# Kernel tuning notes

Hardware: AMD Instinct MI355X
Metric: run time of the kernel (lower is better)

Reference implementation:

```python
import jax, jax.numpy as jnp
import numpy as np

B, S, DM = 1, 2048, 2048
H, KV, DH = 32, 8, 64
ROT, DQ = 32, 16  # rotary dims; DQ = ROT // 2
GROUPS = H // KV


def setup_inputs() -> dict:
    key = jax.random.key(0)
    ks = jax.random.split(key, 9)
    sc = 0.02
    hidden_states = jax.random.normal(ks[0], (B, S, DM), jnp.float32)
    # realistic RoPE tables: theta = pos * inv_freq, shape [1,1,S,DQ] (broadcasts over heads)
    inv_freq = 1.0 / (10000.0 ** (jnp.arange(DQ, dtype=jnp.float32) / DQ))
    ang = jnp.arange(S, dtype=jnp.float32)[:, None] * inv_freq[None, :]
    cos = jnp.cos(ang)[None, None]
    sin = jnp.sin(ang)[None, None]
    position_ids = jnp.broadcast_to(jnp.arange(S, dtype=jnp.int64 if jax.config.read('jax_enable_x64') else jnp.int32), (B, S))
    Wq = jax.random.normal(ks[1], (DM, H * DH), jnp.float32) * sc
    Wk = jax.random.normal(ks[2], (DM, KV * DH), jnp.float32) * sc
    Wv = jax.random.normal(ks[3], (DM, KV * DH), jnp.float32) * sc
    Wo = jax.random.normal(ks[4], (H * DH, DM), jnp.float32) * sc
    qkv_dim = H * DH + 2 * KV * DH
    tau_Wq = jax.random.normal(ks[5], (qkv_dim, H), jnp.float32) * sc
    tau_Wv = jax.random.normal(ks[6], (qkv_dim, H), jnp.float32) * sc
    tau_alpha = jax.random.normal(ks[7], (H,), jnp.float32)
    return {"hidden_states": hidden_states, "cos": cos, "sin": sin,
            "position_ids": position_ids, "Wq": Wq, "Wk": Wk, "Wv": Wv,
            "Wo": Wo, "tau_Wq": tau_Wq, "tau_Wv": tau_Wv, "tau_alpha": tau_alpha}


def _rope(x, cos, sin):
    # x: [B, h, S, DH]; rotate first ROT dims (half-split real/imag), interleave output
    x_rot, x_pass = x[..., :ROT], x[..., ROT:]
    xr, xi = x_rot[..., :DQ], x_rot[..., DQ:]
    out_r = xr * cos - xi * sin
    out_i = xr * sin + xi * cos
    out = jnp.stack([out_r, out_i], axis=-1).reshape(x.shape[:-1] + (ROT,))
    return jnp.concatenate([out, x_pass], axis=-1)


def reference(hidden_states, cos, sin, position_ids, Wq, Wk, Wv, Wo, tau_Wq, tau_Wv, tau_alpha):
    b, s, _ = hidden_states.shape
    q = hidden_states @ Wq                      # [B,S,H*DH]
    k = hidden_states @ Wk                      # [B,S,KV*DH]
    v = hidden_states @ Wv                      # [B,S,KV*DH]
    # tau gating: gelu(concat qkv) -> tanh projections -> position sigmoid term
    feat = jax.nn.gelu(jnp.concatenate([q, k, v], axis=-1), approximate=False)
    tok_q = jnp.tanh(feat @ tau_Wq).transpose(0, 2, 1)   # [B,H,S]
    tok_v = jnp.tanh(feat @ tau_Wv).transpose(0, 2, 1)   # [B,H,S]
    pos = position_ids.astype(hidden_states.dtype) + 1.0
    tau_pos = 1.0 + (jax.nn.sigmoid(tau_alpha[None, :, None] * jnp.log(pos)[:, None, :]) - 0.5)
    tau_q = (tok_q + tau_pos)[..., None]        # [B,H,S,1]
    tau_v = (tok_v + tau_pos)[..., None]        # [B,H,S,1]
    q = q.reshape(b, s, H, DH).transpose(0, 2, 1, 3) * tau_q   # [B,H,S,DH]
    k = k.reshape(b, s, KV, DH).transpose(0, 2, 1, 3)          # [B,KV,S,DH]
    # torch: tau_v.repeat(1,groups,1,1)[:, :KV] == first KV heads of tau_v
    v = v.reshape(b, s, KV, DH).transpose(0, 2, 1, 3) * tau_v[:, :KV]
    q = _rope(q, cos, sin)
    k = _rope(k, cos, sin)
    # GQA expand kv heads, causal SDPA
    k = jnp.repeat(k, GROUPS, axis=1)
    v = jnp.repeat(v, GROUPS, axis=1)
    scores = jnp.einsum('bhqd,bhkd->bhqk', q, k) / np.sqrt(DH).astype(np.float32)
    causal = jnp.tril(jnp.ones((s, s), dtype=bool))
    scores = jnp.where(causal, scores, jnp.finfo(scores.dtype).min)
    attn = jax.nn.softmax(scores, axis=-1)
    out = jnp.einsum('bhqk,bhkd->bhqd', attn, v)
    out = out.transpose(0, 2, 1, 3).reshape(b, s, H * DH)
    return out @ Wo
```

## Files before the change

kernel.cpp:

```cpp
#include <hip/hip_runtime.h>
#include <cmath>

typedef __bf16 bf16x8 __attribute__((ext_vector_type(8)));
typedef __bf16 bf16x4 __attribute__((ext_vector_type(4)));
typedef float f32x4 __attribute__((ext_vector_type(4)));
typedef unsigned short u16;
typedef unsigned int u32;

__device__ __forceinline__ u16 f2bf(float f) {
  union { float f; unsigned int u; } v; v.f = f;
  unsigned int u = v.u;
  return (u16)((u + 0x7FFFu + ((u >> 16) & 1u)) >> 16);
}
__device__ __forceinline__ float bf2f(u16 b) {
  union { u32 u; float f; } v; v.u = ((u32)b) << 16; return v.f;
}

__device__ __forceinline__ float geluf(float x) {
  return 0.5f * x * (1.0f + erff(x * 0.7071067811865475f));
}

__device__ __forceinline__ void gl_lds16(const void* g, void* l) {
  __builtin_amdgcn_global_load_lds(
      (const __attribute__((address_space(1))) u32*)g,
      (__attribute__((address_space(3))) u32*)l, 16, 0, 0);
}

__global__ __launch_bounds__(256) void setup_all(const float* __restrict__ hidden,
                                                 const float* __restrict__ Wq,
                                                 const float* __restrict__ Wk,
                                                 const float* __restrict__ Wv,
                                                 const float* __restrict__ Wo,
                                                 const float* __restrict__ tWq,
                                                 const float* __restrict__ tWv,
                                                 u16* __restrict__ Xb,
                                                 u16* __restrict__ WqkvT,
                                                 u16* __restrict__ WoT,
                                                 u16* __restrict__ Tt) {
  __shared__ float tile[64][65];
  int b = blockIdx.x;
  if (b < 2048) {
    int i = b * 256 + threadIdx.x;
    const float4* p = (const float4*)hidden + 2 * (size_t)i;
    float4 a = p[0], c = p[1];
    uint4 o;
    o.x = (u32)f2bf(a.x) | ((u32)f2bf(a.y) << 16);
    o.y = (u32)f2bf(a.z) | ((u32)f2bf(a.w) << 16);
    o.z = (u32)f2bf(c.x) | ((u32)f2bf(c.y) << 16);
    o.w = (u32)f2bf(c.z) | ((u32)f2bf(c.w) << 16);
    ((uint4*)Xb)[i] = o;
    return;
  }
  b -= 2048;
  const float* in; u16* out; int R, C, bx, by;
  if (b < 1024)      { in = Wq;  out = WqkvT;                R = 2048; C = 2048; bx = b & 31; by = b >> 5; }
  else if (b < 1280) { b -= 1024; in = Wk; out = WqkvT + 2048ull * 2048; R = 2048; C = 512; bx = b & 7; by = b >> 3; }
  else if (b < 1536) { b -= 1280; in = Wv; out = WqkvT + 2560ull * 2048; R = 2048; C = 512; bx = b & 7; by = b >> 3; }
  else if (b < 2560) { b -= 1536; in = Wo; out = WoT;        R = 2048; C = 2048; bx = b & 31; by = b >> 5; }
  else if (b < 2608) { b -= 2560; in = tWq; out = Tt;               R = 3072; C = 32; bx = 0; by = b; }
  else               { b -= 2608; in = tWv; out = Tt + 32ull * 3072; R = 3072; C = 32; bx = 0; by = b; }

  const int t = threadIdx.x;
  const int r0 = by * 64, c0 = bx * 64;
  const int lr = t >> 4, lc4 = (t & 15) * 4;
#pragma unroll
  for (int p = 0; p < 4; ++p) {
    int r = p * 16 + lr;
    float4 v = {0.f, 0.f, 0.f, 0.f};
    if (c0 + lc4 < C) v = *(const float4*)(in + (size_t)(r0 + r) * C + c0 + lc4);
    tile[r][lc4] = v.x; tile[r][lc4 + 1] = v.y;
    tile[r][lc4 + 2] = v.z; tile[r][lc4 + 3] = v.w;
  }
  __syncthreads();
  const int cg = t >> 4, rr4 = (t & 15) * 4;
#pragma unroll
  for (int p = 0; p < 4; ++p) {
    int c = p * 16 + cg;
    if (c0 + c < C) {
      uint2 w;
      w.x = (u32)f2bf(tile[rr4][c])     | ((u32)f2bf(tile[rr4 + 1][c]) << 16);
      w.y = (u32)f2bf(tile[rr4 + 2][c]) | ((u32)f2bf(tile[rr4 + 3][c]) << 16);
      *(uint2*)(out + (size_t)(c0 + c) * R + r0 + rr4) = w;
    }
  }
}

template <int WR, int WC, bool ATOMIC>
__global__ __launch_bounds__(256, 3) void gemm_bt(const u16* __restrict__ A,
                                                  const u16* __restrict__ Bt,
                                                  float* __restrict__ Cpart,
                                                  int M, int N, int K, int kPer) {
  constexpr int BM = WR * 64, BN = WC * 64;
  __shared__ __attribute__((aligned(16))) u16 As[BM * 64];
  __shared__ __attribute__((aligned(16))) u16 Bs[BN * 64];
  const int tid = threadIdx.x, wid = tid >> 6, lane = tid & 63;
  const int l16 = lane & 15, quad = lane >> 4;
  const int wm = (wid % WR) * 64, wn = (wid / WR) * 64;
  const int m0 = blockIdx.y * BM, n0 = blockIdx.x * BN;
  const int kIters = K >> 6;
  const int kStart = blockIdx.z * kPer;
  const int kEnd = (kStart + kPer < kIters) ? (kStart + kPer) : kIters;

  const int lrow = lane >> 3;
  const int swz = (lane & 7) ^ lrow;
  const u16* gAb = A + (size_t)m0 * K + (size_t)swz * 8;
  const u16* gBb = Bt + (size_t)n0 * K + (size_t)swz * 8;
  const int sx = l16 & 7;

  f32x4 acc[4][4] = {};
  for (int kt = kStart; kt < kEnd; ++kt) {
    __syncthreads();
    const u16* gA = gAb + (size_t)kt * 64;
    const u16* gB = gBb + (size_t)kt * 64;
#pragma unroll
    for (int j = 0; j < BM / 32; ++j) {
      int i = wid * (BM / 32) + j;
      gl_lds16(gA + (size_t)(i * 8 + lrow) * K, &As[i * 512]);
    }
#pragma unroll
    for (int j = 0; j < BN / 32; ++j) {
      int i = wid * (BN / 32) + j;
      gl_lds16(gB + (size_t)(i * 8 + lrow) * K, &Bs[i * 512]);
    }
    __syncthreads();
    bf16x8 af[4][2], bfr[4][2];
#pragma unroll
    for (int mt = 0; mt < 4; ++mt)
#pragma unroll
      for (int ks = 0; ks < 2; ++ks)
        af[mt][ks] = *(const bf16x8*)(&As[(wm + mt * 16 + l16) * 64 +
                                          (((ks * 4 + quad) ^ sx) * 8)]);
#pragma unroll
    for (int nt = 0; nt < 4; ++nt)
#pragma unroll
      for (int ks = 0; ks < 2; ++ks)
        bfr[nt][ks] = *(const bf16x8*)(&Bs[(wn + nt * 16 + l16) * 64 +
                                           (((ks * 4 + quad) ^ sx) * 8)]);
#pragma unroll
    for (int mt = 0; mt < 4; ++mt)
#pragma unroll
      for (int nt = 0; nt < 4; ++nt)
#pragma unroll
        for (int ks = 0; ks < 2; ++ks)
          acc[mt][nt] = __builtin_amdgcn_mfma_f32_16x16x32_bf16(
              af[mt][ks], bfr[nt][ks], acc[mt][nt], 0, 0, 0);
  }

  float* C = ATOMIC ? Cpart : Cpart + (size_t)blockIdx.z * M * N;
#pragma unroll
  for (int mt = 0; mt < 4; ++mt)
#pragma unroll
    for (int nt = 0; nt < 4; ++nt)
#pragma unroll
      for (int r = 0; r < 4; ++r) {
        int row = m0 + wm + mt * 16 + quad * 4 + r;
        int col = n0 + wn + nt * 16 + l16;
        if constexpr (ATOMIC)
          unsafeAtomicAdd(&C[(size_t)row * N + col], acc[mt][nt][r]);
        else
          C[(size_t)row * N + col] = acc[mt][nt][r];
      }
}

__global__ __launch_bounds__(256) void reduce_gelu(float* __restrict__ base, int P,
                                                   int n4, u16* __restrict__ gout) {
  int i = blockIdx.x * 256 + threadIdx.x;
  if (i >= n4) return;
  size_t n = (size_t)n4 * 4;
  float4 v = ((const float4*)base)[i];
  for (int p = 1; p < P; ++p) {
    float4 w = ((const float4*)(base + (size_t)p * n))[i];
    v.x += w.x; v.y += w.y; v.z += w.z; v.w += w.w;
  }
  if (P > 1) ((float4*)base)[i] = v;
  uint2 o;
  o.x = (u32)f2bf(geluf(v.x)) | ((u32)f2bf(geluf(v.y)) << 16);
  o.y = (u32)f2bf(geluf(v.z)) | ((u32)f2bf(geluf(v.w)) << 16);
  ((uint2*)gout)[i] = o;
}

#define QSCALE 0.18033688011112042f
__global__ __launch_bounds__(256) void prep_qkv(const float* __restrict__ qkv,
                                                const float* __restrict__ tokPart,
                                                int P,
                                                const float* __restrict__ alpha,
                                                const float* __restrict__ cosb,
                                                const float* __restrict__ sinb,
                                                const int* __restrict__ pos_ids,
                                                u16* __restrict__ Qb,
                                                u16* __restrict__ Kb,
                                                u16* __restrict__ Vt,
                                                u16* __restrict__ Vb) {
  const int s = blockIdx.x;
  const int tid = threadIdx.x;
  __shared__ float cs[16], sn[16], tk[64], tq_s[32], tv_s[32];
  if (tid < 16) { cs[tid] = cosb[s * 16 + tid]; sn[tid] = sinb[s * 16 + tid]; }
  if (tid >= 64 && tid < 128) {
    int c = tid - 64;
    float v = 0.f;
    for (int p = 0; p < P; ++p) v += tokPart[(size_t)p * 2048 * 64 + s * 64 + c];
    tk[c] = tanhf(v);
  }
  __syncthreads();
  if (tid < 32) {
    float p = (float)pos_ids[s] + 1.0f;
    float sig = 1.0f / (1.0f + __expf(-alpha[tid] * logf(p)));
    float taupos = 0.5f + sig;
    tq_s[tid] = (tk[tid] + taupos) * QSCALE;
    tv_s[tid] = tk[tid + 32] + taupos;
  }
  __syncthreads();
  const float* row = qkv + (size_t)s * 3072;

  for (int idx = tid; idx < 2048; idx += 256) {
    int h = idx >> 6, d = idx & 63;
    float tq = tq_s[h];
    float v;
    if (d < 32) {
      int i = d >> 1;
      float xr = row[h * 64 + i] * tq, xi = row[h * 64 + 16 + i] * tq;
      v = (d & 1) ? (xr * sn[i] + xi * cs[i]) : (xr * cs[i] - xi * sn[i]);
    } else v = row[h * 64 + d] * tq;
    Qb[((size_t)h * 2048 + s) * 64 + d] = f2bf(v);
  }
  for (int idx = tid; idx < 512; idx += 256) {
    int h = idx >> 6, d = idx & 63;
    const float* kr = row + 2048;
    float v;
    if (d < 32) {
      int i = d >> 1;
      float xr = kr[h * 64 + i], xi = kr[h * 64 + 16 + i];
      v = (d & 1) ? (xr * sn[i] + xi * cs[i]) : (xr * cs[i] - xi * sn[i]);
    } else v = kr[h * 64 + d];
    Kb[((size_t)h * 2048 + s) * 64 + d] = f2bf(v);
  }
  for (int idx = tid; idx < 512; idx += 256) {
    int h = idx >> 6, d = idx & 63;
    float v = row[2560 + h * 64 + d] * tv_s[h];
    u16 b = f2bf(v);
    if (Vb) Vb[((size_t)h * 2048 + s) * 64 + d] = b;
    else    Vt[((size_t)h * 64 + d) * 2048 + s] = b;
  }
}

__global__ __launch_bounds__(256) void vtrans(const u16* __restrict__ Vb,
                                              u16* __restrict__ Vt) {
  __shared__ u16 t[64][68];
  const int s0 = blockIdx.x * 64, h = blockIdx.y;
  const int tid = threadIdx.x;
  const u16* src = Vb + ((size_t)h * 2048 + s0) * 64;
#pragma unroll
  for (int p = 0; p < 4; ++p) {
    int v = p * 256 + tid;
    int r = v >> 4, c = (v & 15) * 4;
    uint2 w = *(const uint2*)(src + (size_t)r * 64 + c);
    t[r][c] = (u16)(w.x & 0xffff); t[r][c + 1] = (u16)(w.x >> 16);
    t[r][c + 2] = (u16)(w.y & 0xffff); t[r][c + 3] = (u16)(w.y >> 16);
  }
  __syncthreads();
  u16* dst = Vt + (size_t)h * 64 * 2048 + s0;
#pragma unroll
  for (int p = 0; p < 4; ++p) {
    int v = p * 256 + tid;
    int d = v >> 4, s = (v & 15) * 4;
    uint2 w;
    w.x = (u32)t[s][d] | ((u32)t[s + 1][d] << 16);
    w.y = (u32)t[s + 2][d] | ((u32)t[s + 3][d] << 16);
    *(uint2*)(dst + (size_t)d * 2048 + s) = w;
  }
}

__global__ __launch_bounds__(256, 3) void flash_attn(const u16* __restrict__ Qb,
                                                     const u16* __restrict__ Kb,
                                                     const u16* __restrict__ Vt,
                                                     u16* __restrict__ Opart,
                                                     float* __restrict__ ml) {
  __shared__ __attribute__((aligned(16))) u16 KsB[2][4096];
  __shared__ __attribute__((aligned(16))) u16 VsB[2][4096];
  __shared__ __attribute__((aligned(16))) u16 Ps[128 * 64];
  const int e = 50 - blockIdx.x;
  const int h = blockIdx.y, kvh = h >> 2;
  int a = 0;
  while (3 * (a + 1) * (a + 2) / 2 <= e) ++a;
  const int rem = e - 3 * a * (a + 1) / 2;
  const int qb = 3 * a + rem / (a + 1);
  const int cc = rem % (a + 1);
  const int k0 = cc * 6;
  const int kvTend = 2 * qb + 2;
  const int k1 = (k0 + 6 < kvTend) ? (k0 + 6) : kvTend;
  const int pid = h * 51 + e;

  const int tid = threadIdx.x, wid = tid >> 6, lane = tid & 63;
  const int l16 = lane & 15, quad = lane >> 4;
  const int lrow = lane >> 3, swz = (lane & 7) ^ lrow, sx = l16 & 7;

  const int q0 = qb * 128 + wid * 32;
  bf16x8 qf[2][2];
#pragma unroll
  for (int mt = 0; mt < 2; ++mt)
#pragma unroll
    for (int ks = 0; ks < 2; ++ks)
      qf[mt][ks] = *(const bf16x8*)(Qb + ((size_t)h * 2048 + q0 + mt * 16 + l16) * 64 +
                                    ks * 32 + quad * 8);

  f32x4 oacc[2][4] = {};
  float mrun[2] = {-3e38f, -3e38f};
  float lrun[2] = {0.f, 0.f};

  const u16* kgb = Kb + ((size_t)kvh * 2048) * 64;
  const u16* vgb = Vt + (size_t)kvh * 64 * 2048;

#define FA_STAGE(KT, BUF)                                                         \
  {                                                                               \
    const u16* kg_ = kgb + (size_t)(KT)*64 * 64;                                  \
    const u16* vg_ = vgb + (size_t)(KT)*64;                                       \
    _Pragma("unroll") for (int j = 0; j < 2; ++j) {                               \
      int i_ = wid * 2 + j;                                                       \
      gl_lds16(kg_ + (size_t)(i_ * 8 + lrow) * 64 + swz * 8, &KsB[BUF][i_ * 512]);\
      gl_lds16(vg_ + (size_t)(i_ * 8 + lrow) * 2048 + swz * 8, &VsB[BUF][i_ * 512]);\
    }                                                                             \
  }

  FA_STAGE(k0, 0)
  for (int kt = k0; kt < k1; ++kt) {
    const int cur = (kt - k0) & 1;
    __syncthreads();
    if (kt + 1 < k1) FA_STAGE(kt + 1, cur ^ 1)
    const u16* Ks = KsB[cur];
    const u16* Vs = VsB[cur];

    f32x4 sacc[2][4] = {};
#pragma unroll
    for (int kf = 0; kf < 4; ++kf) {
      bf16x8 a0 = *(const bf16x8*)(Ks + (kf * 16 + l16) * 64 + ((quad ^ sx) << 3));
      bf16x8 a1 = *(const bf16x8*)(Ks + (kf * 16 + l16) * 64 + (((4 + quad) ^ sx) << 3));
      sacc[0][kf] = __builtin_amdgcn_mfma_f32_16x16x32_bf16(a0, qf[0][0], sacc[0][kf], 0, 0, 0);
      sacc[0][kf] = __builtin_amdgcn_mfma_f32_16x16x32_bf16(a1, qf[0][1], sacc[0][kf], 0, 0, 0);
      sacc[1][kf] = __builtin_amdgcn_mfma_f32_16x16x32_bf16(a0, qf[1][0], sacc[1][kf], 0, 0, 0);
      sacc[1][kf] = __builtin_amdgcn_mfma_f32_16x16x32_bf16(a1, qf[1][1], sacc[1][kf], 0, 0, 0);
    }

    const bool msk = (kt >= 2 * qb);
#pragma unroll
    for (int mt = 0; mt < 2; ++mt) {
      const int qg = q0 + mt * 16 + l16;
      if (msk) {
        const int kb = kt * 64 + quad * 4;
#pragma unroll
        for (int kf = 0; kf < 4; ++kf)
#pragma unroll
          for (int r = 0; r < 4; ++r)
            if (kb + kf * 16 + r > qg) sacc[mt][kf][r] = -1e9f;
      }
      f32x4 m4 = sacc[mt][0];
      m4 = __builtin_elementwise_max(m4, sacc[mt][1]);
      m4 = __builtin_elementwise_max(m4, sacc[mt][2]);
      m4 = __builtin_elementwise_max(m4, sacc[mt][3]);
      float mx = fmaxf(fmaxf(m4[0], m4[1]), fmaxf(m4[2], m4[3]));
      mx = fmaxf(mx, __shfl_xor(mx, 16));
      mx = fmaxf(mx, __shfl_xor(mx, 32));
      float mn = fmaxf(mrun[mt], mx);
      float al = __builtin_amdgcn_exp2f(mrun[mt] - mn);
      mrun[mt] = mn;
      float ps = 0.f;
      const int prow = wid * 32 + mt * 16 + l16;
      u16* prp = Ps + prow * 64 + ((quad & 1) << 2);
      const int pswz = prow & 7;
#pragma unroll
      for (int kf = 0; kf < 4; ++kf) {
        bf16x4 pk;
#pragma unroll
        for (int r = 0; r < 4; ++r) {
          float p = __builtin_amdgcn_exp2f(sacc[mt][kf][r] - mn);
          ps += p;
          pk[r] = (__bf16)p;
        }
        *(bf16x4*)(prp + (((kf * 2 + (quad >> 1)) ^ pswz) << 3)) = pk;
      }
      ps += __shfl_xor(ps, 16);
      ps += __shfl_xor(ps, 32);
      lrun[mt] = lrun[mt] * al + ps;
#pragma unroll
      for (int df = 0; df < 4; ++df) oacc[mt][df] *= al;
    }

#pragma unroll
    for (int ks = 0; ks < 2; ++ks) {
      const int q0r = wid * 32 + l16, q1r = q0r + 16;
      bf16x8 b0 = *(const bf16x8*)(Ps + q0r * 64 + (((ks * 4 + quad) ^ (q0r & 7)) << 3));
      bf16x8 b1 = *(const bf16x8*)(Ps + q1r * 64 + (((ks * 4 + quad) ^ (q1r & 7)) << 3));
#pragma unroll
      for (int df = 0; df < 4; ++df) {
        bf16x8 va = *(const bf16x8*)(Vs + (df * 16 + l16) * 64 + (((ks * 4 + quad) ^ sx) << 3));
        oacc[0][df] = __builtin_amdgcn_mfma_f32_16x16x32_bf16(va, b0, oacc[0][df], 0, 0, 0);
        oacc[1][df] = __builtin_amdgcn_mfma_f32_16x16x32_bf16(va, b1, oacc[1][df], 0, 0, 0);
      }
    }
  }
#undef FA_STAGE

  u16* Op = Opart + (size_t)pid * 128 * 64;
#pragma unroll
  for (int mt = 0; mt < 2; ++mt) {
    const int qrow = wid * 32 + mt * 16 + l16;
#pragma unroll
    for (int df = 0; df < 4; ++df) {
      uint2 pk;
      pk.x = (u32)f2bf(oacc[mt][df][0]) | ((u32)f2bf(oacc[mt][df][1]) << 16);
      pk.y = (u32)f2bf(oacc[mt][df][2]) | ((u32)f2bf(oacc[mt][df][3]) << 16);
      *(uint2*)(Op + (size_t)qrow * 64 + df * 16 + quad * 4) = pk;
    }
    if (quad == 0) {
      ml[((size_t)pid * 128 + qrow) * 2] = mrun[mt];
      ml[((size_t)pid * 128 + qrow) * 2 + 1] = lrun[mt];
    }
  }
}

__global__ __launch_bounds__(256) void fa_combine(const u16* __restrict__ Opart,
                                                  const float* __restrict__ ml,
                                                  u16* __restrict__ Ob) {
  const int qb = blockIdx.x, h = blockIdx.y;
  const int C = (2 * qb + 7) / 6;
  const int aa = qb / 3, bb = qb % 3;
  const int base = h * 51 + 3 * aa * (aa + 1) / 2 + bb * (aa + 1);
  const int t = threadIdx.x;
#pragma unroll
  for (int u = 0; u < 8; ++u) {
    int unit = u * 256 + t;
    int row = unit >> 4, d4 = unit & 15;
    float mstar = -3e38f;
    for (int c = 0; c < C; ++c)
      mstar = fmaxf(mstar, ml[((size_t)(base + c) * 128 + row) * 2]);
    float4 o = {0.f, 0.f, 0.f, 0.f};
    float lsum = 0.f;
    for (int c = 0; c < C; ++c) {
      const float* mlp = &ml[((size_t)(base + c) * 128 + row) * 2];
      float w = __builtin_amdgcn_exp2f(mlp[0] - mstar);
      uint2 v = *(const uint2*)(Opart + ((size_t)(base + c) * 128 + row) * 64 + d4 * 4);
      o.x += w * bf2f((u16)(v.x & 0xffff)); o.y += w * bf2f((u16)(v.x >> 16));
      o.z += w * bf2f((u16)(v.y & 0xffff)); o.w += w * bf2f((u16)(v.y >> 16));
      lsum += w * mlp[1];
    }
    float inv = 1.0f / lsum;
    uint2 pk;
    pk.x = (u32)f2bf(o.x * inv) | ((u32)f2bf(o.y * inv) << 16);
    pk.y = (u32)f2bf(o.z * inv) | ((u32)f2bf(o.w * inv) << 16);
    *(uint2*)(Ob + (size_t)(qb * 128 + row) * 2048 + h * 64 + d4 * 4) = pk;
  }
}

extern "C" void kernel_launch(void* const* d_in, const int* in_sizes, int n_in,
                              void* d_out, int out_size, void* d_ws, size_t ws_size,
                              hipStream_t stream) {
  (void)in_sizes; (void)n_in; (void)out_size;
  const float* hidden = (const float*)d_in[0];
  const float* cosb   = (const float*)d_in[1];
  const float* sinb   = (const float*)d_in[2];
  const int*   pos    = (const int*)d_in[3];
  const float* Wq     = (const float*)d_in[4];
  const float* Wk     = (const float*)d_in[5];
  const float* Wv     = (const float*)d_in[6];
  const float* Wo     = (const float*)d_in[7];
  const float* tWq    = (const float*)d_in[8];
  const float* tWv    = (const float*)d_in[9];
  const float* alpha  = (const float*)d_in[10];
  float* out = (float*)d_out;

  const bool big = ws_size >= (size_t)120 * 1024 * 1024;
  const int Pq = big ? 2 : 1;
  const int Pt = big ? 16 : 1;
  const int Po = big ? 3 : 1;

  char* ws = (char*)d_ws;
  size_t off = 0;
  auto alloc = [&](size_t bytes) -> void* {
    void* p = ws + off;
    off += (bytes + 255) & ~(size_t)255;
    return p;
  };
  u16*   WoT   = (u16*)alloc(2048ull * 2048 * 2);
  u16*   Tt    = (u16*)alloc(64ull * 3072 * 2);
  u16*   Qb    = (u16*)alloc(32ull * 2048 * 64 * 2);
  u16*   Kb    = (u16*)alloc(8ull * 2048 * 64 * 2);
  u16*   Vt    = (u16*)alloc(8ull * 64 * 2048 * 2);
  u16*   Ob    = (u16*)alloc(2048ull * 2048 * 2);
  u16*   featb = (u16*)alloc(2048ull * 3072 * 2);
  u16*   Vb    = big ? (u16*)alloc(8ull * 2048 * 64 * 2) : nullptr;
  size_t E = off;
  u16*   Xb      = (u16*)alloc(2048ull * 2048 * 2);
  u16*   WqkvT   = (u16*)alloc(3072ull * 2048 * 2);
  float* qkvPart = (float*)alloc((size_t)Pq * 2048 * 3072 * 4);
  float* qkv     = qkvPart;
  float* tokPart = (float*)(ws + E);
  u16*   Opart   = (u16*)(ws + E);
  float* mlbuf   = (float*)(ws + E + 1632ull * 128 * 64 * 2);

  setup_all<<<4704, 256, 0, stream>>>(hidden, Wq, Wk, Wv, Wo, tWq, tWv,
                                      Xb, WqkvT, WoT, Tt);

  gemm_bt<2, 2, false><<<dim3(24, 16, Pq), 256, 0, stream>>>(
      Xb, WqkvT, qkvPart, 2048, 3072, 2048, (32 + Pq - 1) / Pq);
  reduce_gelu<<<6144, 256, 0, stream>>>(qkvPart, Pq, 2048 * 3072 / 4, featb);

  gemm_bt<4, 1, false><<<dim3(1, 8, Pt), 256, 0, stream>>>(
      featb, Tt, tokPart, 2048, 64, 3072, (48 + Pt - 1) / Pt);

  prep_qkv<<<2048, 256, 0, stream>>>(qkv, tokPart, Pt, alpha, cosb, sinb, pos,
                                     Qb, Kb, Vt, Vb);
  if (big) vtrans<<<dim3(32, 8), 256, 0, stream>>>(Vb, Vt);

  flash_attn<<<dim3(51, 32), 256, 0, stream>>>(Qb, Kb, Vt, Opart, mlbuf);
  fa_combine<<<dim3(16, 32), 256, 0, stream>>>(Opart, mlbuf, Ob);

  hipMemsetAsync(out, 0, 2048ull * 2048 * 4, stream);
  gemm_bt<2, 2, true><<<dim3(16, 16, Po), 256, 0, stream>>>(
      Ob, WoT, out, 2048, 2048, 2048, (32 + Po - 1) / Po);
}
```

Measured before the change: 317.4 us.

## Double-buffer GEMM LDS tiles and replace atomic output with partial-sum reduction

The bf16 GEMM now keeps two LDS buffers for A and B. It issues the async global-to-LDS loads for the next k-tile before the MFMA work on the current tile, which drops one barrier per iteration and overlaps memory traffic with compute. LDS use doubles, so launch bounds fall from 3 to 2 blocks per SM, cutting occupancy. The final output projection no longer memsets the output and accumulates split-K results with float atomics. It writes per-split partial buffers into the workspace and sums them in a new reduce_add kernel. That costs extra memory traffic and one more launch, but avoids atomic contention.

```diff
diff --git a/kernel.cpp b/kernel.cpp
--- a/kernel.cpp
+++ b/kernel.cpp
@@ -85,14 +85,14 @@
   }
 }
 
-template <int WR, int WC, bool ATOMIC>
-__global__ __launch_bounds__(256, 3) void gemm_bt(const u16* __restrict__ A,
+template <int WR, int WC>
+__global__ __launch_bounds__(256, 2) void gemm_bt(const u16* __restrict__ A,
                                                   const u16* __restrict__ Bt,
                                                   float* __restrict__ Cpart,
                                                   int M, int N, int K, int kPer) {
   constexpr int BM = WR * 64, BN = WC * 64;
-  __shared__ __attribute__((aligned(16))) u16 As[BM * 64];
-  __shared__ __attribute__((aligned(16))) u16 Bs[BN * 64];
+  __shared__ __attribute__((aligned(16))) u16 AsB[2][BM * 64];
+  __shared__ __attribute__((aligned(16))) u16 BsB[2][BN * 64];
   const int tid = threadIdx.x, wid = tid >> 6, lane = tid & 63;
   const int l16 = lane & 15, quad = lane >> 4;
   const int wm = (wid % WR) * 64, wn = (wid / WR) * 64;
@@ -107,22 +107,28 @@
   const u16* gBb = Bt + (size_t)n0 * K + (size_t)swz * 8;
   const int sx = l16 & 7;
 
+#define GB_STAGE(KT, BUF)                                                      \
+  {                                                                            \
+    const u16* gA_ = gAb + (size_t)(KT)*64;                                    \
+    const u16* gB_ = gBb + (size_t)(KT)*64;                                    \
+    _Pragma("unroll") for (int j = 0; j < BM / 32; ++j) {                      \
+      int i_ = wid * (BM / 32) + j;                                            \
+      gl_lds16(gA_ + (size_t)(i_ * 8 + lrow) * K, &AsB[BUF][i_ * 512]);        \
+    }                                                                          \
+    _Pragma("unroll") for (int j = 0; j < BN / 32; ++j) {                      \
+      int i_ = wid * (BN / 32) + j;                                            \
+      gl_lds16(gB_ + (size_t)(i_ * 8 + lrow) * K, &BsB[BUF][i_ * 512]);        \
+    }                                                                          \
+  }
+
   f32x4 acc[4][4] = {};
+  GB_STAGE(kStart, 0)
   for (int kt = kStart; kt < kEnd; ++kt) {
+    const int cur = (kt - kStart) & 1;
     __syncthreads();
-    const u16* gA = gAb + (size_t)kt * 64;
-    const u16* gB = gBb + (size_t)kt * 64;
-#pragma unroll
-    for (int j = 0; j < BM / 32; ++j) {
-      int i = wid * (BM / 32) + j;
-      gl_lds16(gA + (size_t)(i * 8 + lrow) * K, &As[i * 512]);
-    }
-#pragma unroll
-    for (int j = 0; j < BN / 32; ++j) {
-      int i = wid * (BN / 32) + j;
-      gl_lds16(gB + (size_t)(i * 8 + lrow) * K, &Bs[i * 512]);
-    }
-    __syncthreads();
+    if (kt + 1 < kEnd) GB_STAGE(kt + 1, cur ^ 1)
+    const u16* As = AsB[cur];
+    const u16* Bs = BsB[cur];
     bf16x8 af[4][2], bfr[4][2];
 #pragma unroll
     for (int mt = 0; mt < 4; ++mt)
@@ -145,8 +151,9 @@
           acc[mt][nt] = __builtin_amdgcn_mfma_f32_16x16x32_bf16(
               af[mt][ks], bfr[nt][ks], acc[mt][nt], 0, 0, 0);
   }
-
-  float* C = ATOMIC ? Cpart : Cpart + (size_t)blockIdx.z * M * N;
+#undef GB_STAGE
+
+  float* C = Cpart + (size_t)blockIdx.z * M * N;
 #pragma unroll
   for (int mt = 0; mt < 4; ++mt)
 #pragma unroll
@@ -155,10 +162,7 @@
       for (int r = 0; r < 4; ++r) {
         int row = m0 + wm + mt * 16 + quad * 4 + r;
         int col = n0 + wn + nt * 16 + l16;
-        if constexpr (ATOMIC)
-          unsafeAtomicAdd(&C[(size_t)row * N + col], acc[mt][nt][r]);
-        else
-          C[(size_t)row * N + col] = acc[mt][nt][r];
+        C[(size_t)row * N + col] = acc[mt][nt][r];
       }
 }
 
@@ -177,6 +181,19 @@
   o.x = (u32)f2bf(geluf(v.x)) | ((u32)f2bf(geluf(v.y)) << 16);
   o.y = (u32)f2bf(geluf(v.z)) | ((u32)f2bf(geluf(v.w)) << 16);
   ((uint2*)gout)[i] = o;
+}
+
+__global__ __launch_bounds__(256) void reduce_add(const float* __restrict__ base, int P,
+                                                  int n4, float* __restrict__ dst) {
+  int i = blockIdx.x * 256 + threadIdx.x;
+  if (i >= n4) return;
+  size_t n = (size_t)n4 * 4;
+  float4 v = ((const float4*)base)[i];
+  for (int p = 1; p < P; ++p) {
+    float4 w = ((const float4*)(base + (size_t)p * n))[i];
+    v.x += w.x; v.y += w.y; v.z += w.z; v.w += w.w;
+  }
+  ((float4*)dst)[i] = v;
 }
 
 #define QSCALE 0.18033688011112042f
@@ -495,15 +512,16 @@
   float* tokPart = (float*)(ws + E);
   u16*   Opart   = (u16*)(ws + E);
   float* mlbuf   = (float*)(ws + E + 1632ull * 128 * 64 * 2);
+  float* outPart = (float*)(ws + E);
 
   setup_all<<<4704, 256, 0, stream>>>(hidden, Wq, Wk, Wv, Wo, tWq, tWv,
                                       Xb, WqkvT, WoT, Tt);
 
-  gemm_bt<2, 2, false><<<dim3(24, 16, Pq), 256, 0, stream>>>(
+  gemm_bt<2, 2><<<dim3(24, 16, Pq), 256, 0, stream>>>(
       Xb, WqkvT, qkvPart, 2048, 3072, 2048, (32 + Pq - 1) / Pq);
   reduce_gelu<<<6144, 256, 0, stream>>>(qkvPart, Pq, 2048 * 3072 / 4, featb);
 
-  gemm_bt<4, 1, false><<<dim3(1, 8, Pt), 256, 0, stream>>>(
+  gemm_bt<4, 1><<<dim3(1, 8, Pt), 256, 0, stream>>>(
       featb, Tt, tokPart, 2048, 64, 3072, (48 + Pt - 1) / Pt);
 
   prep_qkv<<<2048, 256, 0, stream>>>(qkv, tokPart, Pt, alpha, cosb, sinb, pos,
@@ -513,7 +531,7 @@
   flash_attn<<<dim3(51, 32), 256, 0, stream>>>(Qb, Kb, Vt, Opart, mlbuf);
   fa_combine<<<dim3(16, 32), 256, 0, stream>>>(Opart, mlbuf, Ob);
 
-  hipMemsetAsync(out, 0, 2048ull * 2048 * 4, stream);
-  gemm_bt<2, 2, true><<<dim3(16, 16, Po), 256, 0, stream>>>(
-      Ob, WoT, out, 2048, 2048, 2048, (32 + Po - 1) / Po);
-}
+  gemm_bt<2, 2><<<dim3(16, 16, Po), 256, 0, stream>>>(
+      Ob, WoT, outPart, 2048, 2048, 2048, (32 + Po - 1) / Po);
+  reduce_add<<<4096, 256, 0, stream>>>(outPart, Po, 2048 * 2048 / 4, out);
+}
```

New measurement: 298.1 us. 1.06x faster.
